# Performance work log

Measured on AMD Instinct MI355X. Metric: run time of the kernel, lower is better.

Reference implementation:

```python
import jax, jax.numpy as jnp
import numpy as np

MASK_VAL = -50000.0
N_HEADS = 16

def setup_inputs() -> dict:
    key = jax.random.key(0)
    k1, k2, k3, k4 = jax.random.split(key, 4)
    b, n, d = 2, 2048, 1024
    s = d ** -0.5  # xavier-ish scale for weights
    return {
        "x": jax.random.normal(k1, (b, n, d), dtype=jnp.float32),
        "Wq": jax.random.normal(k2, (d, d), dtype=jnp.float32) * s,
        "Wkv": jax.random.normal(k3, (d, 2 * d), dtype=jnp.float32) * s,
        "Wo": jax.random.normal(k4, (d, d), dtype=jnp.float32) * s,
    }

def reference(x, Wq, Wkv, Wo):
    b, n, d = x.shape
    h = N_HEADS
    hd = d // h
    scale = hd ** -0.5
    # in-projection
    q = x @ Wq                      # [b, n, d]
    kv = x @ Wkv                    # [b, n, 2d]
    k, v = jnp.split(kv, 2, axis=-1)
    # split heads: b n (h d) -> b h n d
    split = lambda t: t.reshape(b, n, h, hd).transpose(0, 2, 1, 3)
    q, k, v = split(q), split(k), split(v)
    # scaled dot-product scores
    dots = jnp.einsum('bhid,bhjd->bhij', q * scale, k)  # [b, h, n, n]
    # causal mask: upper triangle (j > i) set to MASK_VAL (not -inf, per source)
    causal = jnp.triu(jnp.ones((n, n), dtype=bool), 1)
    dots = jnp.where(causal, MASK_VAL, dots)
    attn = jax.nn.softmax(dots, axis=-1)
    out = jnp.einsum('bhij,bhjd->bhid', attn, v)
    out = out.transpose(0, 2, 1, 3).reshape(b, n, d)  # merge heads
    return out @ Wo
```

## Files before the change

kernel.cpp:

```cpp
#include <hip/hip_runtime.h>
#include <stdint.h>
#include <stddef.h>


typedef __bf16 bf16;
typedef __bf16 bf16x8 __attribute__((ext_vector_type(8)));
typedef __bf16 bf16x4 __attribute__((ext_vector_type(4)));
typedef __bf16 bf16x2 __attribute__((ext_vector_type(2)));
typedef float  f32x4  __attribute__((ext_vector_type(4)));
typedef float  f32x16 __attribute__((ext_vector_type(16)));

#define NSEQ 2048
#define DM   1024
#define HD   64
#define QKVS 3072
#define LOG2E 1.44269504f

#define GLD16(g, l) __builtin_amdgcn_global_load_lds(                         \
    (const __attribute__((address_space(1))) void*)(g),                       \
    (__attribute__((address_space(3))) void*)(l), 16, 0, 0)

__global__ void detect_dtype(const uint32_t* __restrict__ x, int* __restrict__ flag) {
  __shared__ int cnt;
  if (threadIdx.x == 0) cnt = 0;
  __syncthreads();
  int c = 0;
  for (int i = threadIdx.x; i < 4096; i += 256) {
    uint32_t e = (x[i] >> 7) & 0xFF;
    if (e >= 110 && e <= 132) c++;
  }
  atomicAdd(&cnt, c);
  __syncthreads();
  if (threadIdx.x == 0) *flag = (cnt > 2048) ? 1 : 0;
}

__global__ __launch_bounds__(256) void convert_x(
    const void* __restrict__ in, bf16* __restrict__ out, int n,
    const int* __restrict__ flagp) {
  const int flag = *flagp;
  const int i = (blockIdx.x * 256 + threadIdx.x) * 8;
  if (i >= n) return;
  if (flag) {
    *(bf16x8*)(out + i) = *(const bf16x8*)((const bf16*)in + i);
  } else {
    const float* f = (const float*)in;
    bf16x8 v;
#pragma unroll
    for (int e = 0; e < 8; ++e) v[e] = (bf16)f[i + e];
    *(bf16x8*)(out + i) = v;
  }
}

__global__ void transpose_conv(const void* __restrict__ in, bf16* __restrict__ out,
                               int K, int N, const int* __restrict__ flagp) {
  __shared__ bf16 tile[32][33];
  const int flag = *flagp;
  const int k0 = blockIdx.y * 32, n0 = blockIdx.x * 32;
  const int tx = threadIdx.x, ty = threadIdx.y;
  if (flag) {
    const bf16* p = (const bf16*)in;
#pragma unroll
    for (int i = ty; i < 32; i += 8)
      tile[i][tx] = p[(size_t)(k0 + i) * N + n0 + tx];
  } else {
    const float* p = (const float*)in;
#pragma unroll
    for (int i = ty; i < 32; i += 8)
      tile[i][tx] = (bf16)p[(size_t)(k0 + i) * N + n0 + tx];
  }
  __syncthreads();
#pragma unroll
  for (int i = ty; i < 32; i += 8)
    out[(size_t)(n0 + i) * K + k0 + tx] = tile[tx][i];
}

__global__ __launch_bounds__(256) void gemm_bt(
    const bf16* __restrict__ A, const bf16* __restrict__ Bt,
    void* __restrict__ C, int M, int N, int K, const int* flagp)
{
  __shared__ bf16 As[128][64];
  __shared__ bf16 Bs[128][64];
  const int tid  = threadIdx.x;
  const int wave = tid >> 6, lane = tid & 63;
  const int fr = lane & 15, fg = lane >> 4;
  const int m0 = blockIdx.y * 128, n0 = blockIdx.x * 128;
  const int wr = (wave >> 1) * 64, wc = (wave & 1) * 64;
  const int lrow = lane >> 3;
  const int lcol = 8 * ((lane & 7) ^ lrow);

  f32x4 acc[4][4] = {};

  for (int kt = 0; kt < K; kt += 64) {
    __syncthreads();
#pragma unroll
    for (int p = 0; p < 4; ++p) {
      const int chunk = wave * 4 + p;
      const int r = chunk * 8 + lrow;
      GLD16(A  + (size_t)(m0 + r) * K + kt + lcol, &As[chunk * 8][0]);
      GLD16(Bt + (size_t)(n0 + r) * K + kt + lcol, &Bs[chunk * 8][0]);
    }
    __syncthreads();
#pragma unroll
    for (int s = 0; s < 2; ++s) {
      bf16x8 af[4], bfr[4];
#pragma unroll
      for (int i = 0; i < 4; ++i) {
        const int ar = wr + i * 16 + fr;
        af[i]  = *(const bf16x8*)((const char*)&As[ar][0] +
                   ((s * 64 + fg * 16) ^ ((ar & 7) << 4)));
        const int br = wc + i * 16 + fr;
        bfr[i] = *(const bf16x8*)((const char*)&Bs[br][0] +
                   ((s * 64 + fg * 16) ^ ((br & 7) << 4)));
      }
#pragma unroll
      for (int i = 0; i < 4; ++i)
#pragma unroll
        for (int j = 0; j < 4; ++j)
          acc[i][j] = __builtin_amdgcn_mfma_f32_16x16x32_bf16(
              af[i], bfr[j], acc[i][j], 0, 0, 0);
    }
  }
  const int crow = m0 + wr + fg * 4;
  const int ccol = n0 + wc + fr;
  const int as_bf16 = flagp ? *flagp : 1;
  if (as_bf16) {
    bf16* Cb = (bf16*)C;
#pragma unroll
    for (int i = 0; i < 4; ++i)
#pragma unroll
      for (int j = 0; j < 4; ++j)
#pragma unroll
        for (int r = 0; r < 4; ++r)
          Cb[(size_t)(crow + i * 16 + r) * N + ccol + j * 16] = (bf16)acc[i][j][r];
  } else {
    float* Cf = (float*)C;
#pragma unroll
    for (int i = 0; i < 4; ++i)
#pragma unroll
      for (int j = 0; j < 4; ++j)
#pragma unroll
        for (int r = 0; r < 4; ++r)
          Cf[(size_t)(crow + i * 16 + r) * N + ccol + j * 16] = acc[i][j][r];
  }
}

static __device__ inline uint32_t pk2(float a, float b) {
  bf16x2 t; t[0] = (bf16)a; t[1] = (bf16)b;
  return __builtin_bit_cast(uint32_t, t);
}

static __device__ __forceinline__ void strip_tile(
    const bf16 (&Ksb)[64][64], const bf16 (&Vtb)[64][64],
    const bf16x8 (&qf)[4], f32x16 (&oacc)[2], float& m, float& l,
    const int j0, const int q0, const int c, const int h)
{
  const int qrow = q0 + c;
  const int blkmax = (j0 + 32 <= q0 + 31) ? 2 : 1;

  f32x16 sv[2];
  __builtin_amdgcn_s_setprio(1);
#pragma unroll
  for (int blk = 0; blk < 2; ++blk)
    if (blk < blkmax) {
      f32x16 a = {};
#pragma unroll
      for (int ks = 0; ks < 4; ++ks) {
        const int krow = blk * 32 + c;
        bf16x8 kf = *(const bf16x8*)((const char*)&Ksb[krow][0] +
                     ((ks * 32 + h * 16) ^ ((krow & 7) << 4)));
        a = __builtin_amdgcn_mfma_f32_32x32x16_bf16(kf, qf[ks], a, 0, 0, 0);
      }
      sv[blk] = a;
    }
  __builtin_amdgcn_s_setprio(0);

  if (j0 + 63 > q0) {
#pragma unroll
    for (int blk = 0; blk < 2; ++blk)
      if (blk < blkmax) {
        const int kvb = j0 + blk * 32 + 4 * h;
#pragma unroll
        for (int r = 0; r < 16; ++r) {
          const int kv = kvb + (r & 3) + 8 * (r >> 2);
          if (kv > qrow) sv[blk][r] = -4.0e8f;
        }
      }
  }

  float tmax = -3.0e38f;
#pragma unroll
  for (int blk = 0; blk < 2; ++blk)
    if (blk < blkmax)
#pragma unroll
      for (int r = 0; r < 16; ++r) tmax = fmaxf(tmax, sv[blk][r]);
  tmax = fmaxf(tmax, __shfl_xor(tmax, 32));
  const float pmax = tmax * 0.125f;
  if (!__all(pmax - m <= 8.0f)) {
    const float mnew  = fmaxf(m, pmax);
    const float alpha = __builtin_amdgcn_exp2f((m - mnew) * LOG2E);
    m = mnew;
    l *= alpha;
#pragma unroll
    for (int db = 0; db < 2; ++db)
#pragma unroll
      for (int r = 0; r < 16; ++r) oacc[db][r] *= alpha;
  }
  const float km = 0.125f * LOG2E, kb = -m * LOG2E;
  float sum = 0.f;
#pragma unroll
  for (int blk = 0; blk < 2; ++blk)
    if (blk < blkmax)
#pragma unroll
      for (int r = 0; r < 16; ++r) {
        const float p = __builtin_amdgcn_exp2f(__builtin_fmaf(sv[blk][r], km, kb));
        sv[blk][r] = p;
        sum += p;
      }
  sum += __shfl_xor(sum, 32);
  l += sum;

#pragma unroll
  for (int blk = 0; blk < 2; ++blk)
    if (blk < blkmax) {
      uint32_t w[8], xw[8];
#pragma unroll
      for (int g = 0; g < 4; ++g) {
        w[2 * g]     = pk2(sv[blk][4 * g],     sv[blk][4 * g + 1]);
        w[2 * g + 1] = pk2(sv[blk][4 * g + 2], sv[blk][4 * g + 3]);
      }
#pragma unroll
      for (int i = 0; i < 8; ++i)
        xw[i] = (uint32_t)__shfl_xor((int)w[i], 32);
#pragma unroll
      for (int ks = 0; ks < 2; ++ks) {
        union { uint32_t u[4]; bf16x8 v; } pf;
        pf.u[0] = h ? xw[4 * ks + 2] : w[4 * ks];
        pf.u[1] = h ? xw[4 * ks + 3] : w[4 * ks + 1];
        pf.u[2] = h ? w[4 * ks + 2]  : xw[4 * ks];
        pf.u[3] = h ? w[4 * ks + 3]  : xw[4 * ks + 1];
        __builtin_amdgcn_s_setprio(1);
#pragma unroll
        for (int db = 0; db < 2; ++db) {
          const int vrow = db * 32 + c;
          bf16x8 vf = *(const bf16x8*)((const char*)&Vtb[vrow][0] +
                       ((blk * 64 + ks * 32 + h * 16) ^ ((vrow & 7) << 4)));
          oacc[db] = __builtin_amdgcn_mfma_f32_32x32x16_bf16(vf, pf.v, oacc[db], 0, 0, 0);
        }
        __builtin_amdgcn_s_setprio(0);
      }
    }
}

__global__ __launch_bounds__(128) void attn_fwd(
    const bf16* __restrict__ QKV, bf16* __restrict__ O)
{
  __shared__ bf16 Ks[2][64][64];
  __shared__ bf16 Vt[2][64][64];

  const int pr = blockIdx.x;
  const int bh = blockIdx.y;
  const int bi = bh >> 4, hi = bh & 15;
  const int tid = threadIdx.x, wave = tid >> 6, lane = tid & 63;
  const int c = lane & 31, h = lane >> 5;

  const bf16* qptr = QKV + (size_t)bi * NSEQ * QKVS + hi * HD;
  const bf16* kptr = qptr + DM;
  const bf16* vptr = qptr + 2 * DM;

  const int sA = 2 * pr + wave, sB = 63 - sA;
  const int q0A = sA * 32, q0B = sB * 32;

  bf16x8 qfA[4], qfB[4];
#pragma unroll
  for (int ks = 0; ks < 4; ++ks) {
    qfA[ks] = *(const bf16x8*)(qptr + (size_t)(q0A + c) * QKVS + ks * 16 + h * 8);
    qfB[ks] = *(const bf16x8*)(qptr + (size_t)(q0B + c) * QKVS + ks * 16 + h * 8);
  }

  f32x16 oaccA[2] = {}, oaccB[2] = {};
  float mA = -1e30f, lA = 0.f, mB = -1e30f, lB = 0.f;

  const int srow = tid >> 3, sch = tid & 7;
  const int koff = (sch * 16) ^ ((srow & 7) << 4);
  const int kvg = (tid & 15) * 4, dg = (tid >> 4) * 8;

  bf16x8 kpre[4], vpre[4];

  const int ntil = 32 - pr;

  {
#pragma unroll
    for (int p = 0; p < 4; ++p)
      kpre[p] = *(const bf16x8*)(kptr + (size_t)(srow + 16 * p) * QKVS + sch * 8);
#pragma unroll
    for (int i = 0; i < 4; ++i)
      vpre[i] = *(const bf16x8*)(vptr + (size_t)(kvg + i) * QKVS + dg);
#pragma unroll
    for (int p = 0; p < 4; ++p)
      *(bf16x8*)((char*)&Ks[0][srow + 16 * p][0] + koff) = kpre[p];
#pragma unroll
    for (int e = 0; e < 8; ++e) {
      const int d = dg + e;
      bf16x4 w; w[0] = vpre[0][e]; w[1] = vpre[1][e];
      w[2] = vpre[2][e]; w[3] = vpre[3][e];
      *(bf16x4*)((char*)&Vt[0][d][0] + ((2 * kvg) ^ ((d & 7) << 4))) = w;
    }
#pragma unroll
    for (int p = 0; p < 4; ++p)
      kpre[p] = *(const bf16x8*)(kptr + (size_t)(64 + srow + 16 * p) * QKVS + sch * 8);
#pragma unroll
    for (int i = 0; i < 4; ++i)
      vpre[i] = *(const bf16x8*)(vptr + (size_t)(64 + kvg + i) * QKVS + dg);
  }
  __syncthreads();

  for (int t = 0; t < ntil; ++t) {
    const int cur = t & 1;
    const int j0 = t * 64;

    if (t + 1 < ntil) {
      const int nb = cur ^ 1;
#pragma unroll
      for (int p = 0; p < 4; ++p)
        *(bf16x8*)((char*)&Ks[nb][srow + 16 * p][0] + koff) = kpre[p];
#pragma unroll
      for (int e = 0; e < 8; ++e) {
        const int d = dg + e;
        bf16x4 w; w[0] = vpre[0][e]; w[1] = vpre[1][e];
        w[2] = vpre[2][e]; w[3] = vpre[3][e];
        *(bf16x4*)((char*)&Vt[nb][d][0] + ((2 * kvg) ^ ((d & 7) << 4))) = w;
      }
    }
    if (t + 2 < ntil) {
      const int jn = j0 + 128;
#pragma unroll
      for (int p = 0; p < 4; ++p)
        kpre[p] = *(const bf16x8*)(kptr + (size_t)(jn + srow + 16 * p) * QKVS + sch * 8);
#pragma unroll
      for (int i = 0; i < 4; ++i)
        vpre[i] = *(const bf16x8*)(vptr + (size_t)(jn + kvg + i) * QKVS + dg);
    }

    strip_tile(Ks[cur], Vt[cur], qfB, oaccB, mB, lB, j0, q0B, c, h);
    if (j0 <= q0A + 31)
      strip_tile(Ks[cur], Vt[cur], qfA, oaccA, mA, lA, j0, q0A, c, h);

    __syncthreads();
  }

#pragma unroll
  for (int sidx = 0; sidx < 2; ++sidx) {
    const f32x16* oacc = sidx ? oaccB : oaccA;
    const float linv = 1.f / (sidx ? lB : lA);
    const int q0 = sidx ? q0B : q0A;
    bf16* obase = O + (size_t)bi * NSEQ * DM + (size_t)hi * HD +
                  (size_t)(q0 + c) * DM;
#pragma unroll
    for (int db = 0; db < 2; ++db)
#pragma unroll
      for (int g = 0; g < 4; ++g) {
        bf16x4 ov;
#pragma unroll
        for (int j = 0; j < 4; ++j) ov[j] = (bf16)(oacc[db][4 * g + j] * linv);
        *(bf16x4*)(obase + db * 32 + 8 * g + 4 * h) = ov;
      }
  }
}

extern "C" void kernel_launch(void* const* d_in, const int* in_sizes, int n_in,
                              void* d_out, int out_size, void* d_ws, size_t ws_size,
                              hipStream_t stream) {
  const void* x   = d_in[0];
  const void* Wq  = d_in[1];
  const void* Wkv = d_in[2];
  const void* Wo  = d_in[3];

  char* ws = (char*)d_ws;
  int*  flag   = (int*)ws;
  bf16* xb     = (bf16*)(ws + (4ull << 10));
  bf16* WqkvT  = (bf16*)(ws + (4ull << 10) + (8ull  << 20));
  bf16* WoT    = (bf16*)(ws + (4ull << 10) + (14ull << 20));
  bf16* QKVb   = (bf16*)(ws + (4ull << 10) + (16ull << 20));
  bf16* AOb    = xb;

  detect_dtype<<<1, 256, 0, stream>>>((const uint32_t*)x, flag);
  convert_x<<<4194304 / 8 / 256, 256, 0, stream>>>(x, xb, 4194304, flag);

  const dim3 tb(32, 8);
  transpose_conv<<<dim3(1024 / 32, 1024 / 32), tb, 0, stream>>>(Wq,  WqkvT,                1024, 1024, flag);
  transpose_conv<<<dim3(2048 / 32, 1024 / 32), tb, 0, stream>>>(Wkv, WqkvT + 1024 * 1024,  1024, 2048, flag);
  transpose_conv<<<dim3(1024 / 32, 1024 / 32), tb, 0, stream>>>(Wo,  WoT,                  1024, 1024, flag);

  gemm_bt<<<dim3(3072 / 128, 4096 / 128), 256, 0, stream>>>(xb, WqkvT, QKVb, 4096, 3072, 1024, nullptr);

  attn_fwd<<<dim3(16, 32), 128, 0, stream>>>(QKVb, AOb);

  gemm_bt<<<dim3(1024 / 128, 4096 / 128), 256, 0, stream>>>(AOb, WoT, d_out, 4096, 1024, 1024, flag);
}
```

Before: 149.2 us.

## Split attention KV loop across two blocks and merge partials in combine kernel

The attention kernel gains a second grid dimension of size two. Each block walks alternating 64-key tiles and writes an unnormalized bf16 partial output plus per-row max and sum. A new attn_combine kernel rescales the two partials with log-sum-exp weights and writes the normalized head output for the output projection. The aim is to double the number of attention blocks and raise occupancy on the many CUs. The cost is an extra launch, roughly 24 MB of extra partial-output traffic, and reuse of workspace buffers and d_out as scratch.

```diff
diff --git a/kernel.cpp b/kernel.cpp
--- a/kernel.cpp
+++ b/kernel.cpp
@@ -252,13 +252,15 @@
 }
 
 __global__ __launch_bounds__(128) void attn_fwd(
-    const bf16* __restrict__ QKV, bf16* __restrict__ O)
+    const bf16* __restrict__ QKV, bf16* __restrict__ O0, bf16* __restrict__ O1,
+    float2* __restrict__ mlbuf)
 {
   __shared__ bf16 Ks[2][64][64];
   __shared__ bf16 Vt[2][64][64];
 
   const int pr = blockIdx.x;
   const int bh = blockIdx.y;
+  const int z  = blockIdx.z;
   const int bi = bh >> 4, hi = bh & 15;
   const int tid = threadIdx.x, wave = tid >> 6, lane = tid & 63;
   const int c = lane & 31, h = lane >> 5;
@@ -289,12 +291,13 @@
   const int ntil = 32 - pr;
 
   {
+    const size_t jz = (size_t)(z * 64);
 #pragma unroll
     for (int p = 0; p < 4; ++p)
-      kpre[p] = *(const bf16x8*)(kptr + (size_t)(srow + 16 * p) * QKVS + sch * 8);
+      kpre[p] = *(const bf16x8*)(kptr + (jz + srow + 16 * p) * QKVS + sch * 8);
 #pragma unroll
     for (int i = 0; i < 4; ++i)
-      vpre[i] = *(const bf16x8*)(vptr + (size_t)(kvg + i) * QKVS + dg);
+      vpre[i] = *(const bf16x8*)(vptr + (jz + kvg + i) * QKVS + dg);
 #pragma unroll
     for (int p = 0; p < 4; ++p)
       *(bf16x8*)((char*)&Ks[0][srow + 16 * p][0] + koff) = kpre[p];
@@ -305,20 +308,23 @@
       w[2] = vpre[2][e]; w[3] = vpre[3][e];
       *(bf16x4*)((char*)&Vt[0][d][0] + ((2 * kvg) ^ ((d & 7) << 4))) = w;
     }
-#pragma unroll
-    for (int p = 0; p < 4; ++p)
-      kpre[p] = *(const bf16x8*)(kptr + (size_t)(64 + srow + 16 * p) * QKVS + sch * 8);
-#pragma unroll
-    for (int i = 0; i < 4; ++i)
-      vpre[i] = *(const bf16x8*)(vptr + (size_t)(64 + kvg + i) * QKVS + dg);
+    if (z + 2 < ntil) {
+      const size_t jn = (size_t)((z + 2) * 64);
+#pragma unroll
+      for (int p = 0; p < 4; ++p)
+        kpre[p] = *(const bf16x8*)(kptr + (jn + srow + 16 * p) * QKVS + sch * 8);
+#pragma unroll
+      for (int i = 0; i < 4; ++i)
+        vpre[i] = *(const bf16x8*)(vptr + (jn + kvg + i) * QKVS + dg);
+    }
   }
   __syncthreads();
 
-  for (int t = 0; t < ntil; ++t) {
-    const int cur = t & 1;
-    const int j0 = t * 64;
-
-    if (t + 1 < ntil) {
+  int cur = 0;
+  for (int j = z; j < ntil; j += 2) {
+    const int j0 = j * 64;
+
+    if (j + 2 < ntil) {
       const int nb = cur ^ 1;
 #pragma unroll
       for (int p = 0; p < 4; ++p)
@@ -331,29 +337,31 @@
         *(bf16x4*)((char*)&Vt[nb][d][0] + ((2 * kvg) ^ ((d & 7) << 4))) = w;
       }
     }
-    if (t + 2 < ntil) {
-      const int jn = j0 + 128;
+    if (j + 4 < ntil) {
+      const size_t jn = (size_t)((j + 4) * 64);
 #pragma unroll
       for (int p = 0; p < 4; ++p)
-        kpre[p] = *(const bf16x8*)(kptr + (size_t)(jn + srow + 16 * p) * QKVS + sch * 8);
+        kpre[p] = *(const bf16x8*)(kptr + (jn + srow + 16 * p) * QKVS + sch * 8);
 #pragma unroll
       for (int i = 0; i < 4; ++i)
-        vpre[i] = *(const bf16x8*)(vptr + (size_t)(jn + kvg + i) * QKVS + dg);
-    }
-
-    strip_tile(Ks[cur], Vt[cur], qfB, oaccB, mB, lB, j0, q0B, c, h);
+        vpre[i] = *(const bf16x8*)(vptr + (jn + kvg + i) * QKVS + dg);
+    }
+
+    if (j0 <= q0B + 31)
+      strip_tile(Ks[cur], Vt[cur], qfB, oaccB, mB, lB, j0, q0B, c, h);
     if (j0 <= q0A + 31)
       strip_tile(Ks[cur], Vt[cur], qfA, oaccA, mA, lA, j0, q0A, c, h);
 
     __syncthreads();
-  }
-
+    cur ^= 1;
+  }
+
+  bf16* Op = z ? O1 : O0;
 #pragma unroll
   for (int sidx = 0; sidx < 2; ++sidx) {
     const f32x16* oacc = sidx ? oaccB : oaccA;
-    const float linv = 1.f / (sidx ? lB : lA);
     const int q0 = sidx ? q0B : q0A;
-    bf16* obase = O + (size_t)bi * NSEQ * DM + (size_t)hi * HD +
+    bf16* obase = Op + (size_t)bi * NSEQ * DM + (size_t)hi * HD +
                   (size_t)(q0 + c) * DM;
 #pragma unroll
     for (int db = 0; db < 2; ++db)
@@ -361,10 +369,41 @@
       for (int g = 0; g < 4; ++g) {
         bf16x4 ov;
 #pragma unroll
-        for (int j = 0; j < 4; ++j) ov[j] = (bf16)(oacc[db][4 * g + j] * linv);
+        for (int jj = 0; jj < 4; ++jj) ov[jj] = (bf16)oacc[db][4 * g + jj];
         *(bf16x4*)(obase + db * 32 + 8 * g + 4 * h) = ov;
       }
-  }
+    if (h == 0) {
+      float2 v; v.x = sidx ? mB : mA; v.y = sidx ? lB : lA;
+      mlbuf[(size_t)(((z * 2 + bi) * 16 + hi)) * NSEQ + q0 + c] = v;
+    }
+  }
+}
+
+__global__ __launch_bounds__(256) void attn_combine(
+    const bf16* __restrict__ O0, const bf16* __restrict__ O1,
+    const float2* __restrict__ mlbuf, bf16* __restrict__ out)
+{
+  const int idx = blockIdx.x * 256 + threadIdx.x;
+  const int e8 = idx * 8;
+  const int qg  = e8 >> 10;
+  const int col = e8 & 1023;
+  const int hi  = col >> 6;
+  const int bi  = qg >> 11;
+  const int q   = qg & 2047;
+  const float2 ml0 = mlbuf[(size_t)(((0 * 2 + bi) * 16 + hi)) * NSEQ + q];
+  const float2 ml1 = mlbuf[(size_t)(((1 * 2 + bi) * 16 + hi)) * NSEQ + q];
+  const float M = fmaxf(ml0.x, ml1.x);
+  const float w0 = __builtin_amdgcn_exp2f((ml0.x - M) * LOG2E);
+  const float w1 = __builtin_amdgcn_exp2f((ml1.x - M) * LOG2E);
+  const float dinv = 1.f / (w0 * ml0.y + w1 * ml1.y);
+  const float s0 = w0 * dinv, s1 = w1 * dinv;
+  bf16x8 a = *(const bf16x8*)(O0 + e8);
+  bf16x8 b = *(const bf16x8*)(O1 + e8);
+  bf16x8 o;
+#pragma unroll
+  for (int e = 0; e < 8; ++e)
+    o[e] = (bf16)(s0 * (float)a[e] + s1 * (float)b[e]);
+  *(bf16x8*)(out + e8) = o;
 }
 
 extern "C" void kernel_launch(void* const* d_in, const int* in_sizes, int n_in,
@@ -376,12 +415,15 @@
   const void* Wo  = d_in[3];
 
   char* ws = (char*)d_ws;
-  int*  flag   = (int*)ws;
-  bf16* xb     = (bf16*)(ws + (4ull << 10));
-  bf16* WqkvT  = (bf16*)(ws + (4ull << 10) + (8ull  << 20));
-  bf16* WoT    = (bf16*)(ws + (4ull << 10) + (14ull << 20));
-  bf16* QKVb   = (bf16*)(ws + (4ull << 10) + (16ull << 20));
-  bf16* AOb    = xb;
+  int*    flag  = (int*)ws;
+  bf16*   xb    = (bf16*)(ws + (4ull << 10));
+  bf16*   WqkvT = (bf16*)(ws + (4ull << 10) + (8ull  << 20));
+  bf16*   WoT   = (bf16*)(ws + (4ull << 10) + (14ull << 20));
+  bf16*   QKVb  = (bf16*)(ws + (4ull << 10) + (16ull << 20));
+  bf16*   Opart0 = xb;
+  bf16*   Opart1 = (bf16*)d_out;
+  float2* mlbuf  = (float2*)WqkvT;
+  bf16*   AOb    = QKVb;
 
   detect_dtype<<<1, 256, 0, stream>>>((const uint32_t*)x, flag);
   convert_x<<<4194304 / 8 / 256, 256, 0, stream>>>(x, xb, 4194304, flag);
@@ -393,7 +435,8 @@
 
   gemm_bt<<<dim3(3072 / 128, 4096 / 128), 256, 0, stream>>>(xb, WqkvT, QKVb, 4096, 3072, 1024, nullptr);
 
-  attn_fwd<<<dim3(16, 32), 128, 0, stream>>>(QKVb, AOb);
+  attn_fwd<<<dim3(16, 32, 2), 128, 0, stream>>>(QKVb, Opart0, Opart1, mlbuf);
+  attn_combine<<<4194304 / 8 / 256, 256, 0, stream>>>(Opart0, Opart1, mlbuf, AOb);
 
   gemm_bt<<<dim3(1024 / 128, 4096 / 128), 256, 0, stream>>>(AOb, WoT, d_out, 4096, 1024, 1024, flag);
 }
```

Result: slower. 169.2 us (+13.4%).
